# Optimization experiments

Measured on AMD Instinct MI355X. Metric: run time of the kernel, lower is better.

The kernel has to match this reference:

```python
import jax, jax.numpy as jnp
import numpy as np

EPS = 0.1        # entropic regularization (self.eps)
THRESH = 0.1     # convergence threshold on sum|u - u1| (self.thresh)
MAX_ITER = 100   # self.max_iter
K = 8            # num_neighbors in get_mask_matrix


def setup_inputs() -> dict:
    key = jax.random.key(0)
    k1, k2, k3 = jax.random.split(key, 3)
    B, N, M = 8, 3000, 3000
    mu = jax.random.uniform(k1, (B, N), dtype=jnp.float32)
    mu = mu / mu.sum(-1, keepdims=True)
    nu = jax.random.uniform(k2, (B, M), dtype=jnp.float32)
    nu = nu / nu.sum(-1, keepdims=True)
    C = jax.random.uniform(k3, (B, N, M), dtype=jnp.float32)
    return {"mu": mu, "nu": nu, "C": C}


def _knn_mask(C, k=K):
    # get_mask_matrix: k smallest per row (dim=1) + k largest per column (dim=0)
    B, N, M = C.shape
    _, ir = jax.lax.top_k(-C, k)                       # [B,N,k] smallest along cols
    row_mask = jnp.zeros(C.shape, C.dtype).at[
        jnp.arange(B)[:, None, None], jnp.arange(N)[None, :, None], ir].set(1.0)
    _, ic = jax.lax.top_k(jnp.swapaxes(C, -1, -2), k)  # [B,M,k] largest along rows
    col_mask = jnp.zeros(C.shape, C.dtype).at[
        jnp.arange(B)[:, None, None], ic, jnp.arange(M)[None, :, None]].set(1.0)
    return ((row_mask + col_mask) > 0).astype(C.dtype)


def _sinkhorn(mu, nu, C, A):
    # log-domain Sinkhorn of get_dist, vectorized over batch with per-sample early stop
    B = mu.shape[0]
    log_mu = jnp.log(mu + 1e-8)
    log_nu = jnp.log(nu + 1e-8)

    def exp_M(u, v):
        return A * jnp.exp((-C + u[:, :, None] + v[:, None, :]) / EPS)

    def step(carry, _):
        u, v, done = carry
        u_new = EPS * (log_mu - jnp.log(1e-8 + exp_M(u, v).sum(-1))) + u
        v_new = EPS * (log_nu - jnp.log(1e-8 + exp_M(u_new, v).sum(-2))) + v
        err = jnp.abs(u_new - u).sum(-1)               # [B]
        u_out = jnp.where(done[:, None], u, u_new)
        v_out = jnp.where(done[:, None], v, v_new)
        done = done | (err < THRESH)
        return (u_out, v_out, done), None

    init = (jnp.zeros_like(mu), jnp.zeros_like(nu), jnp.zeros((B,), dtype=bool))
    (u, v, _), _ = jax.lax.scan(step, init, None, length=MAX_ITER)
    pi = exp_M(u, v)
    return jnp.sum(pi * C, axis=(-2, -1))              # [B]


def reference(mu, nu, C):
    # get_cost_matrix: row-wise L2 normalization (F.normalize p=2 dim=1)
    Cn = C / jnp.maximum(jnp.linalg.norm(C, axis=-1, keepdims=True), 1e-12)
    A = _knn_mask(Cn)
    Cm = A * Cn                                        # C = A.to_dense() * C
    cost = _sinkhorn(mu, nu, Cm, A)
    return cost.mean()                                 # gwd / batch
```

## Files before the change

kernel.cpp:

```cpp
#include <hip/hip_runtime.h>
#include <cfloat>

typedef unsigned long long ull;

constexpr int NB = 8, NN = 3000, NM = 3000, KK = 8;
constexpr int CAP = 48;
constexpr float SCALE   = 14.426950408889634f;
constexpr float UNSCALE = 0.06931471805599453f;
constexpr float THRESH  = 0.1f;
constexpr unsigned DUMMY_PAT = 0x7f7f7f7fu;
constexpr int NCH = 32;

constexpr int BPB  = 8;
constexpr int NBLK = NB * BPB;
constexpr int TPB  = 512;
constexpr int RPB  = NN / BPB;

#if __has_builtin(__builtin_amdgcn_exp2f)
#define FEXP2(x) __builtin_amdgcn_exp2f(x)
#else
#define FEXP2(x) exp2f(x)
#endif
#if __has_builtin(__builtin_amdgcn_logf)
#define FLOG2(x) __builtin_amdgcn_logf(x)
#else
#define FLOG2(x) __log2f(x)
#endif

__device__ __forceinline__ ull aload64(const ull* p) {
  return __hip_atomic_load(p, __ATOMIC_RELAXED, __HIP_MEMORY_SCOPE_AGENT);
}
__device__ __forceinline__ void astore64(ull* p, ull x) {
  __hip_atomic_store(p, x, __ATOMIC_RELAXED, __HIP_MEMORY_SCOPE_AGENT);
}

__device__ __forceinline__ void pull_tagged(const ull* __restrict__ src, int tag,
                                            float* __restrict__ dst, int lane) {
  const int nfull = RPB - 5 * 64;
  unsigned pend = (lane < nfull) ? 0x3Fu : 0x1Fu;
  {
    ull x0 = aload64(&src[lane]);
    ull x1 = aload64(&src[lane + 64]);
    ull x2 = aload64(&src[lane + 128]);
    ull x3 = aload64(&src[lane + 192]);
    ull x4 = aload64(&src[lane + 256]);
    ull x5 = (lane < nfull) ? aload64(&src[lane + 320]) : 0;
    if ((int)(x0 >> 32) == tag) { dst[lane]       = __uint_as_float((unsigned)x0); pend &= ~1u;  }
    if ((int)(x1 >> 32) == tag) { dst[lane + 64]  = __uint_as_float((unsigned)x1); pend &= ~2u;  }
    if ((int)(x2 >> 32) == tag) { dst[lane + 128] = __uint_as_float((unsigned)x2); pend &= ~4u;  }
    if ((int)(x3 >> 32) == tag) { dst[lane + 192] = __uint_as_float((unsigned)x3); pend &= ~8u;  }
    if ((int)(x4 >> 32) == tag) { dst[lane + 256] = __uint_as_float((unsigned)x4); pend &= ~16u; }
    if ((lane < nfull) && (int)(x5 >> 32) == tag) { dst[lane + 320] = __uint_as_float((unsigned)x5); pend &= ~32u; }
  }
  while (pend) {
    __builtin_amdgcn_s_sleep(1);
#pragma unroll
    for (int j = 0; j < 6; ++j) {
      if (!((pend >> j) & 1u)) continue;
      ull x = aload64(&src[lane + 64 * j]);
      if ((int)(x >> 32) == tag) {
        dst[lane + 64 * j] = __uint_as_float((unsigned)x);
        pend &= ~(1u << j);
      }
    }
  }
}

__global__ __launch_bounds__(256) void k_rowprep(const float* __restrict__ C,
                                                 float* __restrict__ invnorms,
                                                 int2* __restrict__ rowsel) {
  const int bn = blockIdx.x * 8 + (threadIdx.x >> 5);
  const int l  = threadIdx.x & 31;
  const float4* row4 = reinterpret_cast<const float4*>(C + (size_t)bn * NM);

  float tv[8]; int ti[8];
#pragma unroll
  for (int q = 0; q < 8; ++q) { tv[q] = FLT_MAX; ti[q] = 0x7fffffff; }
  float sq = 0.f;
  for (int c = 0; c < 24; ++c) {
    int i = l + 32 * c;
    if (i < NM / 4) {
      float4 f = row4[i];
      sq += f.x * f.x + f.y * f.y + f.z * f.z + f.w * f.w;
      float e[4] = { f.x, f.y, f.z, f.w };
#pragma unroll
      for (int j = 0; j < 4; ++j) {
        float v = e[j];
        if (v < tv[7]) {
          int idx = 4 * i + j;
          int pos = 8;
#pragma unroll
          for (int q = 7; q >= 0; --q) if (v < tv[q]) pos = q;
#pragma unroll
          for (int q = 7; q >= 1; --q) if (q > pos) { tv[q] = tv[q-1]; ti[q] = ti[q-1]; }
#pragma unroll
          for (int q = 0; q < 8; ++q) if (q == pos) { tv[q] = v; ti[q] = idx; }
        }
      }
    }
  }
#pragma unroll
  for (int o = 16; o; o >>= 1) sq += __shfl_down(sq, o, 32);

#pragma unroll
  for (int msk = 1; msk <= 16; msk <<= 1) {
    float pv[8]; int pi[8];
#pragma unroll
    for (int q = 0; q < 8; ++q) { pv[q] = __shfl_xor(tv[q], msk); pi[q] = __shfl_xor(ti[q], msk); }
    float mv[8]; int mi[8];
#pragma unroll
    for (int q = 0; q < 8; ++q) {
      float av = tv[q], bv = pv[7 - q];
      int   ai = ti[q], bi = pi[7 - q];
      bool ta = (av < bv) || (av == bv && ai < bi);
      mv[q] = ta ? av : bv; mi[q] = ta ? ai : bi;
    }
    auto ce = [&](int i, int j) {
      bool sw = (mv[i] > mv[j]) || (mv[i] == mv[j] && mi[i] > mi[j]);
      float fv = sw ? mv[j] : mv[i], gv = sw ? mv[i] : mv[j];
      int   fi = sw ? mi[j] : mi[i], gi = sw ? mi[i] : mi[j];
      mv[i] = fv; mv[j] = gv; mi[i] = fi; mi[j] = gi;
    };
    ce(0,4); ce(1,5); ce(2,6); ce(3,7);
    ce(0,2); ce(1,3); ce(4,6); ce(5,7);
    ce(0,1); ce(2,3); ce(4,5); ce(6,7);
#pragma unroll
    for (int q = 0; q < 8; ++q) { tv[q] = mv[q]; ti[q] = mi[q]; }
  }

  if (l == 0) {
#pragma unroll
    for (int q = 0; q < 8; ++q)
      rowsel[(size_t)bn * KK + q] = make_int2(ti[q], __float_as_int(tv[q]));
    float nm = sqrtf(sq);
    invnorms[bn] = 1.0f / fmaxf(nm, 1e-12f);
  }
}

__global__ __launch_bounds__(256) void k_coltop1(const float* __restrict__ C,
                                                 const float* __restrict__ invnorms,
                                                 ull* __restrict__ partial) {
  const int b = blockIdx.z, rc = blockIdx.y, cg = blockIdx.x;
  const int tid = threadIdx.x;
  const int w = tid >> 6, l = tid & 63;
  const int g4 = cg * 64 + l;
  const int chunk = rc * 4 + w;

  ull tv[4][8];
#pragma unroll
  for (int j = 0; j < 4; ++j)
#pragma unroll
    for (int q = 0; q < 8; ++q) tv[j][q] = 0;

  if (g4 < NM / 4) {
    const int base_r = rc * 375;
    const int r0 = base_r + w * 94;
    const int r1 = min(base_r + 375, r0 + 94);
    const float4* base = reinterpret_cast<const float4*>(
        C + (size_t)b * NN * NM) + g4;
    const float* ivn = invnorms + (size_t)b * NN;
    for (int n = r0; n < r1; ++n) {
      float4 f = base[(size_t)n * (NM / 4)];
      float iv = ivn[n];
      float e[4] = { f.x * iv, f.y * iv, f.z * iv, f.w * iv };
      ull lo = (ull)(unsigned)~n;
#pragma unroll
      for (int j = 0; j < 4; ++j) {
        ull key = ((ull)__float_as_uint(e[j]) << 32) | lo;
        if (key > tv[j][7]) {
          int pos = 8;
#pragma unroll
          for (int q = 7; q >= 0; --q) if (key > tv[j][q]) pos = q;
#pragma unroll
          for (int q = 7; q >= 1; --q) if (q > pos) tv[j][q] = tv[j][q-1];
#pragma unroll
          for (int q = 0; q < 8; ++q) if (q == pos) tv[j][q] = key;
        }
      }
    }
    ull* dst = partial + (((size_t)b * NCH + chunk) * NM + (size_t)4 * g4) * 8;
#pragma unroll
    for (int j = 0; j < 4; ++j)
#pragma unroll
      for (int q = 0; q < 8; ++q) dst[j * 8 + q] = tv[j][q];
  }
}

__global__ __launch_bounds__(64) void k_coltop2(const ull* __restrict__ partial,
                                                int2* __restrict__ colsel) {
  int t = blockIdx.x * 64 + threadIdx.x;
  if (t >= NB * NM) return;
  int b = t / NM, m = t % NM;
  ull top[8];
#pragma unroll
  for (int q = 0; q < 8; ++q) top[q] = 0;
  for (int c = 0; c < NCH; ++c) {
    const ull* src = partial + (((size_t)b * NCH + c) * NM + m) * 8;
    ull buf[8];
#pragma unroll
    for (int q = 0; q < 8; ++q) buf[q] = src[q];
    for (int q = 0; q < 8; ++q) {
      ull key = buf[q];
      if (key <= top[7]) break;
      int pos = 8;
#pragma unroll
      for (int z = 7; z >= 0; --z) if (key > top[z]) pos = z;
#pragma unroll
      for (int z = 7; z >= 1; --z) if (z > pos) top[z] = top[z-1];
#pragma unroll
      for (int z = 0; z < 8; ++z) if (z == pos) top[z] = key;
    }
  }
#pragma unroll
  for (int q = 0; q < 8; ++q)
    colsel[(size_t)t * KK + q] =
        make_int2((int)~(unsigned)top[q], (int)(top[q] >> 32));
}

__global__ __launch_bounds__(256) void k_fill(const float* __restrict__ invnorms,
    const int2* __restrict__ rowsel, const int2* __restrict__ colsel,
    int* r_cnt, int* c_cnt, int2* __restrict__ r_pk, int2* __restrict__ c_pk) {
  int t = blockIdx.x * 256 + threadIdx.x;
  if (t >= NB * NN * KK) return;
  int k = t % KK; int bn = t / KK;
  int b = bn / NN; int n = bn % NN;
  float inv_bn = invnorms[bn];
  int2 rs = rowsel[t];
  int2 cs = colsel[t];
  {
    float v2 = __int_as_float(rs.y) * inv_bn * SCALE;
    r_pk[(size_t)bn * CAP + k] = make_int2(rs.x, __float_as_int(v2));
  }
  {
    float v2 = __int_as_float(cs.y) * SCALE;
    c_pk[(size_t)bn * CAP + k] = make_int2(cs.x, __float_as_int(v2));
  }
  int m = n;
  {
    int n3 = cs.x;
    const int2* rl = rowsel + ((size_t)b * NN + n3) * KK;
    bool dup = false;
#pragma unroll
    for (int q = 0; q < KK; ++q) dup |= (rl[q].x == m);
    if (!dup) {
      int slot = 8 + atomicAdd(&r_cnt[(size_t)b * NN + n3], 1);
      if (slot < CAP) {
        float v2 = __int_as_float(cs.y) * SCALE;
        r_pk[((size_t)b * NN + n3) * CAP + slot] = make_int2(m, __float_as_int(v2));
      }
    }
  }
  {
    int mm = rs.x;
    const int2* cl = colsel + ((size_t)b * NM + mm) * KK;
    bool dup = false;
#pragma unroll
    for (int q = 0; q < KK; ++q) dup |= (cl[q].x == n);
    if (!dup) {
      int slot = 8 + atomicAdd(&c_cnt[(size_t)b * NM + mm], 1);
      if (slot < CAP) {
        float v2 = __int_as_float(rs.y) * inv_bn * SCALE;
        c_pk[((size_t)b * NM + mm) * CAP + slot] = make_int2(n, __float_as_int(v2));
      }
    }
  }
}

__global__ __launch_bounds__(TPB, 1) void k_sink_coop(
    const float* __restrict__ mu, const float* __restrict__ nu,
    const int2* __restrict__ r_pk, const int2* __restrict__ c_pk,
    ull* __restrict__ Upub, ull* __restrict__ Vpub,
    ull* errW, float* __restrict__ costpart) {
  const int blk = blockIdx.x;
  const int b = blk % NB, slice = blk / NB;
  const int tid = threadIdx.x;
  const int w = tid >> 6, lane = tid & 63;
  const int r = slice * RPB + tid;
  const bool has_r = (tid < RPB);

  float rval[CAP], cval[CAP];
  unsigned ridx[CAP / 2], cidx[CAP / 2];
  float u = 0.f, vv = 0.f, lmu = 0.f, lnu = 0.f;
  if (has_r) {
    const int2* rp = r_pk + ((size_t)b * NN + r) * CAP;
    const int2* cp = c_pk + ((size_t)b * NM + r) * CAP;
#pragma unroll
    for (int i = 0; i < CAP; i += 2) {
      int2 e0 = rp[i], e1 = rp[i + 1];
      rval[i] = __int_as_float(e0.y); rval[i + 1] = __int_as_float(e1.y);
      unsigned i0 = min((unsigned)e0.x & 0xFFFFu, (unsigned)(NN - 1));
      unsigned i1 = min((unsigned)e1.x & 0xFFFFu, (unsigned)(NN - 1));
      ridx[i / 2] = i0 | (i1 << 16);
      int2 f0 = cp[i], f1 = cp[i + 1];
      cval[i] = __int_as_float(f0.y); cval[i + 1] = __int_as_float(f1.y);
      unsigned j0 = min((unsigned)f0.x & 0xFFFFu, (unsigned)(NN - 1));
      unsigned j1 = min((unsigned)f1.x & 0xFFFFu, (unsigned)(NN - 1));
      cidx[i / 2] = j0 | (j1 << 16);
    }
    lmu = FLOG2(mu[(size_t)b * NN + r] + 1e-8f);
    lnu = FLOG2(nu[(size_t)b * NM + r] + 1e-8f);
  }

  __shared__ float XL[NN];
  __shared__ float sred[TPB / 64];
  __shared__ float errl[BPB];
  int itf = 0;
  bool done = false;

  for (int it = 0; it < 100; ++it) {
    if (it == 0) {
      for (int i = tid; i < NN; i += TPB) XL[i] = 0.f;
    } else {
      if (has_r) XL[r] = vv;
      if (w != slice) {
        const ull* src = Vpub + (size_t)((it - 1) & 1) * (NB * NN)
                       + (size_t)b * NN + (size_t)w * RPB;
        pull_tagged(src, it, XL + w * RPB, lane);
      }
    }
    __syncthreads();

    float errp = 0.f;
    if (has_r) {
      float s = 0.f;
#pragma unroll
      for (int i = 0; i < CAP; ++i) {
        int ix = (ridx[i >> 1] >> ((i & 1) * 16)) & 0xFFFF;
        s += FEXP2(u + XL[ix] - rval[i]);
      }
      float un = lmu - FLOG2(1e-8f + s) + u;
      errp = fabsf(un - u);
      u = un;
      astore64(&Upub[(size_t)(it & 1) * (NB * NN) + (size_t)b * NN + r],
               ((ull)(unsigned)(it + 1) << 32) | __float_as_uint(u));
    }
#pragma unroll
    for (int o = 32; o; o >>= 1) errp += __shfl_down(errp, o);
    if (lane == 0) sred[w] = errp;
    __syncthreads();
    if (tid == 0) {
      float e = sred[0] + sred[1] + sred[2] + sred[3]
              + sred[4] + sred[5] + sred[6] + sred[7];
      astore64(&errW[(size_t)((it & 1) * NB + b) * BPB * 16 + slice * 16],
               ((ull)(unsigned)(it + 1) << 32) | __float_as_uint(e));
      errl[slice] = e;
    }

    if (has_r) XL[r] = u;
    if (w != slice) {
      const ull* src = Upub + (size_t)(it & 1) * (NB * NN)
                     + (size_t)b * NN + (size_t)w * RPB;
      pull_tagged(src, it + 1, XL + w * RPB, lane);
      if (lane == 0) {
        const ull* ep = errW + (size_t)((it & 1) * NB + b) * BPB * 16 + w * 16;
        ull x = aload64(ep);
        while ((int)(x >> 32) != it + 1) { __builtin_amdgcn_s_sleep(1); x = aload64(ep); }
        errl[w] = __uint_as_float((unsigned)x);
      }
    }
    __syncthreads();

    float errtot = errl[0] + errl[1] + errl[2] + errl[3]
                 + errl[4] + errl[5] + errl[6] + errl[7];
    done = (errtot * UNSCALE < THRESH);
    if (has_r) {
      float s = 0.f;
#pragma unroll
      for (int i = 0; i < CAP; ++i) {
        int ix = (cidx[i >> 1] >> ((i & 1) * 16)) & 0xFFFF;
        s += FEXP2(vv + XL[ix] - cval[i]);
      }
      vv = lnu - FLOG2(1e-8f + s) + vv;
      astore64(&Vpub[(size_t)(it & 1) * (NB * NN) + (size_t)b * NN + r],
               ((ull)(unsigned)(it + 1) << 32) | __float_as_uint(vv));
    }
    __syncthreads();
    itf = it;
    if (done) break;
  }

  if (has_r) XL[r] = vv;
  if (w != slice) {
    const ull* src = Vpub + (size_t)(itf & 1) * (NB * NN)
                   + (size_t)b * NN + (size_t)w * RPB;
    pull_tagged(src, itf + 1, XL + w * RPB, lane);
  }
  __syncthreads();
  float cs = 0.f;
  if (has_r) {
#pragma unroll
    for (int i = 0; i < CAP; ++i) {
      int ix = (ridx[i >> 1] >> ((i & 1) * 16)) & 0xFFFF;
      float val = rval[i];
      cs += FEXP2(u + XL[ix] - val) * val;
    }
  }
#pragma unroll
  for (int o = 32; o; o >>= 1) cs += __shfl_down(cs, o);
  if (lane == 0) sred[w] = cs;
  __syncthreads();
  if (tid == 0)
    costpart[b * BPB + slice] = sred[0] + sred[1] + sred[2] + sred[3]
                              + sred[4] + sred[5] + sred[6] + sred[7];
}

__global__ void k_final2(const float* __restrict__ costpart, float* __restrict__ out) {
  if (threadIdx.x == 0 && blockIdx.x == 0) {
    float tot = 0.f;
    for (int b = 0; b < NB; ++b) {
      float cb = 0.f;
      for (int s = 0; s < BPB; ++s) cb += costpart[b * BPB + s];
      tot += cb * UNSCALE;
    }
    out[0] = tot * (1.0f / NB);
  }
}

extern "C" void kernel_launch(void* const* d_in, const int* in_sizes, int n_in,
                              void* d_out, int out_size, void* d_ws, size_t ws_size,
                              hipStream_t stream) {
  const float* mu = (const float*)d_in[0];
  const float* nu = (const float*)d_in[1];
  const float* C  = (const float*)d_in[2];
  float* out = (float*)d_out;

  char* ws = (char*)d_ws;
  size_t off = 0;
  auto alloc = [&](size_t bytes) {
    void* p = ws + off;
    off += (bytes + 255) & ~(size_t)255;
    return p;
  };
  float* invnorms = (float*)alloc(sizeof(float) * NB * NN);
  int2*  rowsel   = (int2*) alloc(sizeof(int2)  * NB * NN * KK);
  int2*  colsel   = (int2*) alloc(sizeof(int2)  * NB * NM * KK);
  ull*   partial  = (ull*)  alloc(sizeof(ull)   * NB * NCH * NM * 8);
  int2*  r_pk     = (int2*) alloc(sizeof(int2)  * NB * NN * CAP);
  int2*  c_pk     = (int2*) alloc(sizeof(int2)  * NB * NM * CAP);
  ull*   Upub     = (ull*)  alloc(sizeof(ull)   * 2 * NB * NN);
  ull*   Vpub     = (ull*)  alloc(sizeof(ull)   * 2 * NB * NM);
  ull*   errW     = (ull*)  alloc(sizeof(ull)   * 2 * NB * BPB * 16);
  int*   r_cnt    = (int*)  alloc(sizeof(int)   * NB * NN);
  int*   c_cnt    = (int*)  alloc(sizeof(int)   * NB * NM);
  float* costpart = (float*)alloc(sizeof(float) * NB * BPB);
  (void)ws_size; (void)in_sizes; (void)n_in; (void)out_size;

  hipMemsetD32Async((hipDeviceptr_t)r_pk, (int)DUMMY_PAT,
                    (size_t)2 * NB * NN * CAP * 2, stream);
  size_t span = (size_t)((char*)costpart - (char*)Upub)
              + ((sizeof(float) * NB * BPB + 255) & ~(size_t)255);
  hipMemsetAsync(Upub, 0, span, stream);

  hipLaunchKernelGGL(k_rowprep, dim3(NB * NN / 8), dim3(256), 0, stream,
                     C, invnorms, rowsel);
  hipLaunchKernelGGL(k_coltop1, dim3(12, NCH / 4, NB), dim3(256), 0, stream,
                     C, invnorms, partial);
  hipLaunchKernelGGL(k_coltop2, dim3((NB * NM + 63) / 64), dim3(64), 0, stream,
                     partial, colsel);
  int nthreads = NB * NN * KK;
  hipLaunchKernelGGL(k_fill, dim3((nthreads + 255) / 256), dim3(256), 0, stream,
                     invnorms, rowsel, colsel, r_cnt, c_cnt, r_pk, c_pk);

  void* args[] = { (void*)&mu, (void*)&nu, (void*)&r_pk, (void*)&c_pk,
                   (void*)&Upub, (void*)&Vpub, (void*)&errW, (void*)&costpart };
  hipLaunchCooperativeKernel((const void*)k_sink_coop, dim3(NBLK), dim3(TPB),
                             args, 0, stream);

  hipLaunchKernelGGL(k_final2, dim3(1), dim3(64), 0, stream, costpart, out);
}
```

Baseline: 830.1 us.

## Fold final reduction into cooperative kernel, move pk fills upstream, halve column chunks

The direct row and column top-k entries of r_pk/c_pk are now written in k_rowprep and k_coltop2, so the fill kernel only handles the cross-inserted extras. The separate final-reduction kernel is removed: block 0 of the cooperative Sinkhorn kernel spin-waits on tagged per-block cost slots and writes the output itself. NCH drops from 32 to 16, giving fewer but longer column-partial chunks and a smaller partial buffer to merge. This saves one launch and some memory traffic, at the cost of a spin-wait in one block and less parallelism in k_coltop1.

```diff
diff --git a/kernel.cpp b/kernel.cpp
--- a/kernel.cpp
+++ b/kernel.cpp
@@ -9,7 +9,7 @@
 constexpr float UNSCALE = 0.06931471805599453f;
 constexpr float THRESH  = 0.1f;
 constexpr unsigned DUMMY_PAT = 0x7f7f7f7fu;
-constexpr int NCH = 32;
+constexpr int NCH = 16;
 
 constexpr int BPB  = 8;
 constexpr int NBLK = NB * BPB;
@@ -68,7 +68,8 @@
 
 __global__ __launch_bounds__(256) void k_rowprep(const float* __restrict__ C,
                                                  float* __restrict__ invnorms,
-                                                 int2* __restrict__ rowsel) {
+                                                 int2* __restrict__ rowsel,
+                                                 int2* __restrict__ r_pk) {
   const int bn = blockIdx.x * 8 + (threadIdx.x >> 5);
   const int l  = threadIdx.x & 31;
   const float4* row4 = reinterpret_cast<const float4*>(C + (size_t)bn * NM);
@@ -129,11 +130,15 @@
   }
 
   if (l == 0) {
-#pragma unroll
-    for (int q = 0; q < 8; ++q)
+    float nm = sqrtf(sq);
+    float inv = 1.0f / fmaxf(nm, 1e-12f);
+    invnorms[bn] = inv;
+#pragma unroll
+    for (int q = 0; q < 8; ++q) {
       rowsel[(size_t)bn * KK + q] = make_int2(ti[q], __float_as_int(tv[q]));
-    float nm = sqrtf(sq);
-    invnorms[bn] = 1.0f / fmaxf(nm, 1e-12f);
+      float v2 = tv[q] * inv * SCALE;
+      r_pk[(size_t)bn * CAP + q] = make_int2(ti[q], __float_as_int(v2));
+    }
   }
 }
 
@@ -153,9 +158,9 @@
     for (int q = 0; q < 8; ++q) tv[j][q] = 0;
 
   if (g4 < NM / 4) {
-    const int base_r = rc * 375;
-    const int r0 = base_r + w * 94;
-    const int r1 = min(base_r + 375, r0 + 94);
+    const int base_r = rc * 750;
+    const int r0 = base_r + w * 188;
+    const int r1 = min(base_r + 750, r0 + 188);
     const float4* base = reinterpret_cast<const float4*>(
         C + (size_t)b * NN * NM) + g4;
     const float* ivn = invnorms + (size_t)b * NN;
@@ -187,7 +192,8 @@
 }
 
 __global__ __launch_bounds__(64) void k_coltop2(const ull* __restrict__ partial,
-                                                int2* __restrict__ colsel) {
+                                                int2* __restrict__ colsel,
+                                                int2* __restrict__ c_pk) {
   int t = blockIdx.x * 64 + threadIdx.x;
   if (t >= NB * NM) return;
   int b = t / NM, m = t % NM;
@@ -212,29 +218,25 @@
     }
   }
 #pragma unroll
-  for (int q = 0; q < 8; ++q)
-    colsel[(size_t)t * KK + q] =
-        make_int2((int)~(unsigned)top[q], (int)(top[q] >> 32));
-}
-
-__global__ __launch_bounds__(256) void k_fill(const float* __restrict__ invnorms,
+  for (int q = 0; q < 8; ++q) {
+    int n = (int)~(unsigned)top[q];
+    int vb = (int)(top[q] >> 32);
+    colsel[(size_t)t * KK + q] = make_int2(n, vb);
+    float v2 = __int_as_float(vb) * SCALE;
+    c_pk[(size_t)t * CAP + q] = make_int2(n, __float_as_int(v2));
+  }
+}
+
+__global__ __launch_bounds__(256) void k_extras(const float* __restrict__ invnorms,
     const int2* __restrict__ rowsel, const int2* __restrict__ colsel,
     int* r_cnt, int* c_cnt, int2* __restrict__ r_pk, int2* __restrict__ c_pk) {
   int t = blockIdx.x * 256 + threadIdx.x;
   if (t >= NB * NN * KK) return;
-  int k = t % KK; int bn = t / KK;
+  int bn = t / KK;
   int b = bn / NN; int n = bn % NN;
   float inv_bn = invnorms[bn];
   int2 rs = rowsel[t];
   int2 cs = colsel[t];
-  {
-    float v2 = __int_as_float(rs.y) * inv_bn * SCALE;
-    r_pk[(size_t)bn * CAP + k] = make_int2(rs.x, __float_as_int(v2));
-  }
-  {
-    float v2 = __int_as_float(cs.y) * SCALE;
-    c_pk[(size_t)bn * CAP + k] = make_int2(cs.x, __float_as_int(v2));
-  }
   int m = n;
   {
     int n3 = cs.x;
@@ -270,7 +272,7 @@
     const float* __restrict__ mu, const float* __restrict__ nu,
     const int2* __restrict__ r_pk, const int2* __restrict__ c_pk,
     ull* __restrict__ Upub, ull* __restrict__ Vpub,
-    ull* errW, float* __restrict__ costpart) {
+    ull* errW, ull* costW, float* __restrict__ out) {
   const int blk = blockIdx.x;
   const int b = blk % NB, slice = blk / NB;
   const int tid = threadIdx.x;
@@ -399,17 +401,32 @@
   for (int o = 32; o; o >>= 1) cs += __shfl_down(cs, o);
   if (lane == 0) sred[w] = cs;
   __syncthreads();
-  if (tid == 0)
-    costpart[b * BPB + slice] = sred[0] + sred[1] + sred[2] + sred[3]
-                              + sred[4] + sred[5] + sred[6] + sred[7];
-}
-
-__global__ void k_final2(const float* __restrict__ costpart, float* __restrict__ out) {
-  if (threadIdx.x == 0 && blockIdx.x == 0) {
+  if (tid == 0) {
+    float tot = sred[0] + sred[1] + sred[2] + sred[3]
+              + sred[4] + sred[5] + sred[6] + sred[7];
+    astore64(&costW[b * BPB + slice], (1ull << 32) | __float_as_uint(tot));
+  }
+
+  if (blk == 0 && tid == 0) {
+    float vals[NB * BPB];
+    unsigned pend_hi = 0xFFFFFFFFu, pend_lo = 0xFFFFFFFFu;
+    for (;;) {
+      bool all = true;
+      for (int i = 0; i < NB * BPB; ++i) {
+        unsigned bit = 1u << (i & 31);
+        unsigned& pw = (i < 32) ? pend_lo : pend_hi;
+        if (!(pw & bit)) continue;
+        ull x = aload64(&costW[i]);
+        if ((int)(x >> 32) == 1) { vals[i] = __uint_as_float((unsigned)x); pw &= ~bit; }
+        else all = false;
+      }
+      if (all && !pend_lo && !pend_hi) break;
+      __builtin_amdgcn_s_sleep(2);
+    }
     float tot = 0.f;
-    for (int b = 0; b < NB; ++b) {
+    for (int bb = 0; bb < NB; ++bb) {
       float cb = 0.f;
-      for (int s = 0; s < BPB; ++s) cb += costpart[b * BPB + s];
+      for (int s = 0; s < BPB; ++s) cb += vals[bb * BPB + s];
       tot += cb * UNSCALE;
     }
     out[0] = tot * (1.0f / NB);
@@ -442,29 +459,28 @@
   ull*   errW     = (ull*)  alloc(sizeof(ull)   * 2 * NB * BPB * 16);
   int*   r_cnt    = (int*)  alloc(sizeof(int)   * NB * NN);
   int*   c_cnt    = (int*)  alloc(sizeof(int)   * NB * NM);
-  float* costpart = (float*)alloc(sizeof(float) * NB * BPB);
+  ull*   costW    = (ull*)  alloc(sizeof(ull)   * NB * BPB);
   (void)ws_size; (void)in_sizes; (void)n_in; (void)out_size;
 
   hipMemsetD32Async((hipDeviceptr_t)r_pk, (int)DUMMY_PAT,
                     (size_t)2 * NB * NN * CAP * 2, stream);
-  size_t span = (size_t)((char*)costpart - (char*)Upub)
-              + ((sizeof(float) * NB * BPB + 255) & ~(size_t)255);
+  size_t span = (size_t)((char*)costW - (char*)Upub)
+              + ((sizeof(ull) * NB * BPB + 255) & ~(size_t)255);
   hipMemsetAsync(Upub, 0, span, stream);
 
   hipLaunchKernelGGL(k_rowprep, dim3(NB * NN / 8), dim3(256), 0, stream,
-                     C, invnorms, rowsel);
+                     C, invnorms, rowsel, r_pk);
   hipLaunchKernelGGL(k_coltop1, dim3(12, NCH / 4, NB), dim3(256), 0, stream,
                      C, invnorms, partial);
   hipLaunchKernelGGL(k_coltop2, dim3((NB * NM + 63) / 64), dim3(64), 0, stream,
-                     partial, colsel);
+                     partial, colsel, c_pk);
   int nthreads = NB * NN * KK;
-  hipLaunchKernelGGL(k_fill, dim3((nthreads + 255) / 256), dim3(256), 0, stream,
+  hipLaunchKernelGGL(k_extras, dim3((nthreads + 255) / 256), dim3(256), 0, stream,
                      invnorms, rowsel, colsel, r_cnt, c_cnt, r_pk, c_pk);
 
   void* args[] = { (void*)&mu, (void*)&nu, (void*)&r_pk, (void*)&c_pk,
-                   (void*)&Upub, (void*)&Vpub, (void*)&errW, (void*)&costpart };
+                   (void*)&Upub, (void*)&Vpub, (void*)&errW, (void*)&costW,
+                   (void*)&out };
   hipLaunchCooperativeKernel((const void*)k_sink_coop, dim3(NBLK), dim3(TPB),
                              args, 0, stream);
-
-  hipLaunchKernelGGL(k_final2, dim3(1), dim3(64), 0, stream, costpart, out);
-}
+}
```

Measured after the change: 898.5 us. +8.2%, slower.
